# Kernel tuning notes

Measured on AMD Instinct MI355X. Metric: run time of the kernel, lower is better.

The kernel has to match this reference:

```python
import jax, jax.numpy as jnp
import numpy as np

N = 100000       # nodes
E = 3200000      # edges
IN_DIM = 128
EDGE_DIM = 16
H = 64           # hidden_dim
L = 3            # num_layers
G = 256          # num graphs
BN_EPS = 1e-5


def setup_inputs() -> dict:
    key = jax.random.key(0)
    ks = jax.random.split(key, 16)
    x = jax.random.normal(ks[0], (N, IN_DIM), dtype=jnp.float32)
    edge_attr = jax.random.normal(ks[1], (E, EDGE_DIM), dtype=jnp.float32)
    edge_index = jax.random.randint(ks[2], (2, E), 0, N, dtype=jnp.int64)
    batch = jnp.sort(jax.random.randint(ks[3], (N,), 0, G, dtype=jnp.int64))
    s = 0.05
    np_w = jax.random.normal(ks[4], (IN_DIM, H), dtype=jnp.float32) * s
    np_b = jnp.zeros((H,), dtype=jnp.float32)
    ep_w = jax.random.normal(ks[5], (EDGE_DIM, H), dtype=jnp.float32) * s
    ep_b = jnp.zeros((H,), dtype=jnp.float32)
    mlp_w1 = jax.random.normal(ks[6], (L, H, H), dtype=jnp.float32) * s
    mlp_b1 = jnp.zeros((L, H), dtype=jnp.float32)
    mlp_w2 = jax.random.normal(ks[7], (L, H, H), dtype=jnp.float32) * s
    mlp_b2 = jnp.zeros((L, H), dtype=jnp.float32)
    bn_g = jnp.ones((L, H), dtype=jnp.float32)
    bn_b = jnp.zeros((L, H), dtype=jnp.float32)
    return {"x": x, "edge_attr": edge_attr, "edge_index": edge_index, "batch": batch,
            "np_w": np_w, "np_b": np_b, "ep_w": ep_w, "ep_b": ep_b,
            "mlp_w1": mlp_w1, "mlp_b1": mlp_b1, "mlp_w2": mlp_w2, "mlp_b2": mlp_b2,
            "bn_g": bn_g, "bn_b": bn_b}


def reference(x, edge_attr, edge_index, batch, np_w, np_b, ep_w, ep_b,
              mlp_w1, mlp_b1, mlp_w2, mlp_b2, bn_g, bn_b):
    h = x @ np_w + np_b                  # [N,H] node_proj
    e = edge_attr @ ep_w + ep_b          # [E,H] edge_proj
    src, dst = edge_index[0], edge_index[1]
    for l in range(L):
        # GINEConv (eps=0): MLP(x_i + sum_j ReLU(x_j + e_ij))
        msg = jax.nn.relu(h[src] + e)                          # [E,H] gather + edge add
        agg = jax.ops.segment_sum(msg, dst, num_segments=N)    # scatter-add
        z = h + agg
        z = jax.nn.relu(z @ mlp_w1[l] + mlp_b1[l]) @ mlp_w2[l] + mlp_b2[l]
        # BatchNorm1d over node dim (batch statistics, training-mode math)
        mu = jnp.mean(z, axis=0)
        var = jnp.mean((z - mu) ** 2, axis=0)
        z = (z - mu) * jax.lax.rsqrt(var + BN_EPS) * bn_g[l] + bn_b[l]
        h = jax.nn.relu(z)               # dropout omitted (deterministic reference)
    # global_mean_pool
    sums = jax.ops.segment_sum(h, batch, num_segments=G)
    cnts = jax.ops.segment_sum(jnp.ones((N,), dtype=h.dtype), batch, num_segments=G)
    graph_emb = sums / jnp.maximum(cnts, 1.0)[:, None]
    return h, graph_emb
```

## Files before the change

kernel.cpp:

```cpp
#include <hip/hip_runtime.h>
#include <hip/hip_bf16.h>

#define NN 100000
#define NE 3200000
#define IND 128
#define ED 16
#define HD 64
#define NL 3
#define NG 256
#define BN_EPS 1e-5f

#define NB 391
#define PBLK 512
#define PCHUNK 6250
#define MLP_BLOCKS 2048
#define APPLY_BLOCKS 2048

typedef unsigned int uint32;
typedef unsigned long long uint64;
typedef unsigned short ushort16;

__device__ __forceinline__ ushort16 f2b(float f) {
    uint32 u = __float_as_uint(f);
    u = (u + 0x7fffu + ((u >> 16) & 1u)) >> 16;
    return (ushort16)u;
}
__device__ __forceinline__ float b2f(ushort16 b) {
    return __uint_as_float(((uint32)b) << 16);
}

__global__ __launch_bounds__(256) void k_node_proj(
    const float* __restrict__ x, const float* __restrict__ w,
    const float* __restrict__ b, ushort16* __restrict__ sb)
{
    __shared__ float xs[4][IND];
    const int wave = threadIdx.x >> 6, lane = threadIdx.x & 63;
    const int node = blockIdx.x * 4 + wave;
    const float2 v = *(const float2*)(x + (size_t)node * IND + lane * 2);
    ((float2*)xs[wave])[lane] = v;
    float acc = b[lane];
#pragma unroll
    for (int k = 0; k < IND; ++k)
        acc = fmaf(xs[wave][k], w[k * HD + lane], acc);
    sb[node * HD + lane] = f2b(acc);
}

__global__ __launch_bounds__(256) void k_p1(const int* __restrict__ ei,
                                            int* __restrict__ bh)
{
    __shared__ int hist[NB];
    const int t = threadIdx.x, blk = blockIdx.x;
    for (int i = t; i < NB; i += 256) hist[i] = 0;
    __syncthreads();
    const int base = blk * PCHUNK;
    for (int i = t; i < PCHUNK; i += 256)
        atomicAdd(&hist[ei[NE + base + i] >> 8], 1);
    __syncthreads();
    for (int i = t; i < NB; i += 256) bh[blk * NB + i] = hist[i];
}

__global__ __launch_bounds__(512) void k_p2(int* __restrict__ bh,
                                            int* __restrict__ bstart,
                                            int* __restrict__ rowptr)
{
    __shared__ int tot[NB];
    __shared__ int bsl[NB + 1];
    const int t = threadIdx.x;
    if (t < NB) {
        int s = 0;
        for (int blk = 0; blk < PBLK; ++blk) {
            const int idx = blk * NB + t;
            const int v = bh[idx];
            bh[idx] = s;
            s += v;
        }
        tot[t] = s;
    }
    __syncthreads();
    if (t == 0) {
        int run = 0;
        for (int b = 0; b < NB; ++b) { bsl[b] = run; run += tot[b]; }
        bsl[NB] = run;
    }
    __syncthreads();
    if (t < NB) {
        const int base = bsl[t];
        for (int blk = 0; blk < PBLK; ++blk) bh[blk * NB + t] += base;
        bstart[t] = base;
    }
    if (t == 0) { bstart[NB] = NE; rowptr[NN] = NE; }
}

__global__ __launch_bounds__(256) void k_p3(const int* __restrict__ ei,
                                            const int* __restrict__ bh,
                                            uint64* __restrict__ tmp)
{
    __shared__ int cursor[NB];
    const int t = threadIdx.x, blk = blockIdx.x;
    for (int i = t; i < NB; i += 256) cursor[i] = bh[blk * NB + i];
    __syncthreads();
    const int base = blk * PCHUNK;
    for (int i = t; i < PCHUNK; i += 256) {
        const int e = base + i;
        const int d = ei[NE + e];
        const int s = ei[e];
        const int pos = atomicAdd(&cursor[d >> 8], 1);
        tmp[pos] = (uint64)(uint32)d | ((uint64)(uint32)s << 17)
                 | ((uint64)(uint32)e << 34);
    }
}

__global__ __launch_bounds__(256) void k_p4(const uint64* __restrict__ tmp,
                                            const int* __restrict__ bstart,
                                            int2* __restrict__ perm_se,
                                            int* __restrict__ rowptr)
{
    __shared__ int cnt[256], csave[256], cnt2[256];
    const int t = threadIdx.x, b = blockIdx.x;
    const int lo = bstart[b], hi = bstart[b + 1];
    cnt[t] = 0; cnt2[t] = 0;
    __syncthreads();
    for (int e = lo + t; e < hi; e += 256)
        atomicAdd(&cnt[(int)(tmp[e] & 0x1FFFF) & 255], 1);
    __syncthreads();
    csave[t] = cnt[t];
    __syncthreads();
    for (int off = 1; off < 256; off <<= 1) {
        const int v = (t >= off) ? cnt[t - off] : 0;
        __syncthreads();
        cnt[t] += v;
        __syncthreads();
    }
    const int excl = cnt[t] - csave[t];
    const int node = (b << 8) + t;
    if (node < NN) rowptr[node] = lo + excl;
    __syncthreads();
    csave[t] = excl;
    __syncthreads();
    for (int e = lo + t; e < hi; e += 256) {
        const uint64 u = tmp[e];
        const int loc = (int)(u & 0x1FFFF) & 255;
        const int r = atomicAdd(&cnt2[loc], 1);
        const int pos = lo + csave[loc] + r;
        perm_se[pos] = make_int2((int)((u >> 17) & 0x1FFFF), (int)(u >> 34));
    }
}

__global__ __launch_bounds__(256) void k_permute(
    const float* __restrict__ ea, const int2* __restrict__ perm_se,
    ushort16* __restrict__ ea_perm)
{
    const int pos = blockIdx.x * 256 + threadIdx.x;
    const int p = pos >> 2, q = pos & 3;
    const int eid = perm_se[p].y;
    const float4 v = ((const float4*)(ea + (size_t)eid * ED))[q];
    ushort4 o;
    o.x = f2b(v.x); o.y = f2b(v.y); o.z = f2b(v.z); o.w = f2b(v.w);
    ((ushort4*)ea_perm)[pos] = o;
}

template <bool XFORM>
__global__ __launch_bounds__(256) void k_gather(
    const ushort16* __restrict__ eab, const int2* __restrict__ perm_se,
    const int* __restrict__ rowptr,
    const float* __restrict__ epw, const float* __restrict__ epb,
    const ushort16* __restrict__ sb, const float* __restrict__ bnp,
    float* __restrict__ z)
{
    const int lane = threadIdx.x & 63;
    float wr[ED];
#pragma unroll
    for (int k = 0; k < ED; ++k) wr[k] = epw[k * HD + lane];
    const float bc = epb[lane];
    const float tsc = XFORM ? bnp[lane] : 1.f;
    const float tsh = XFORM ? bnp[64 + lane] : 0.f;

    const int node = __builtin_amdgcn_readfirstlane((blockIdx.x << 2) + (threadIdx.x >> 6));
    const int rs = rowptr[node];
    const int re = rowptr[node + 1];

    float acc = 0.f;
    int j = rs;
    for (; j + 8 <= re; j += 8) {
        int s[8];
#pragma unroll
        for (int m = 0; m < 8; ++m) s[m] = perm_se[j + m].x;
        float hv[8];
#pragma unroll
        for (int m = 0; m < 8; ++m) {
            float v = b2f(sb[(size_t)s[m] * HD + lane]);
            if (XFORM) v = fmaxf(fmaf(v, tsc, tsh), 0.f);
            hv[m] = v;
        }
#pragma unroll
        for (int m = 0; m < 8; ++m) {
            const uint32* r = (const uint32*)(eab + (size_t)(j + m) * ED);
            float e = bc;
#pragma unroll
            for (int k2 = 0; k2 < ED / 2; ++k2) {
                const uint32 u = r[k2];
                e = fmaf(__uint_as_float(u << 16), wr[2 * k2], e);
                e = fmaf(__uint_as_float(u & 0xffff0000u), wr[2 * k2 + 1], e);
            }
            acc += fmaxf(hv[m] + e, 0.f);
        }
    }
    for (; j < re; ++j) {
        float v = b2f(sb[(size_t)perm_se[j].x * HD + lane]);
        if (XFORM) v = fmaxf(fmaf(v, tsc, tsh), 0.f);
        const uint32* r = (const uint32*)(eab + (size_t)j * ED);
        float e = bc;
#pragma unroll
        for (int k2 = 0; k2 < ED / 2; ++k2) {
            const uint32 u = r[k2];
            e = fmaf(__uint_as_float(u << 16), wr[2 * k2], e);
            e = fmaf(__uint_as_float(u & 0xffff0000u), wr[2 * k2 + 1], e);
        }
        acc += fmaxf(v + e, 0.f);
    }
    float u0 = b2f(sb[(size_t)node * HD + lane]);
    if (XFORM) u0 = fmaxf(fmaf(u0, tsc, tsh), 0.f);
    z[node * HD + lane] = acc + u0;
}

template <bool STORE_BF16>
__global__ __launch_bounds__(256) void k_mlp(
    float* __restrict__ z,
    const float* __restrict__ w1, const float* __restrict__ b1,
    const float* __restrict__ w2, const float* __restrict__ b2,
    ushort16* __restrict__ sb, float* __restrict__ part)
{
    __shared__ float z0s[4][HD];
    __shared__ float t1s[4][HD];
    __shared__ float red[4][2][HD];
    const int wave = threadIdx.x >> 6, lane = threadIdx.x & 63;
    const float vb1 = b1[lane], vb2 = b2[lane];
    float s1 = 0.f, s2 = 0.f;
    for (int node = blockIdx.x * 4 + wave; node < NN; node += MLP_BLOCKS * 4) {
        const int idx = node * HD + lane;
        z0s[wave][lane] = z[idx];
        float a = vb1;
#pragma unroll
        for (int k = 0; k < HD; ++k)
            a = fmaf(z0s[wave][k], w1[k * HD + lane], a);
        a = fmaxf(a, 0.f);
        t1s[wave][lane] = a;
        float o = vb2;
#pragma unroll
        for (int k = 0; k < HD; ++k)
            o = fmaf(t1s[wave][k], w2[k * HD + lane], o);
        if (STORE_BF16) sb[idx] = f2b(o);
        else            z[idx] = o;
        s1 += o;
        s2 += o * o;
    }
    red[wave][0][lane] = s1;
    red[wave][1][lane] = s2;
    __syncthreads();
    if (wave == 0) {
        float a = red[0][0][lane] + red[1][0][lane] + red[2][0][lane] + red[3][0][lane];
        float c = red[0][1][lane] + red[1][1][lane] + red[2][1][lane] + red[3][1][lane];
        part[blockIdx.x * 128 + lane] = a;
        part[blockIdx.x * 128 + 64 + lane] = c;
    }
}

__global__ __launch_bounds__(1024) void k_bn_final(
    const float* __restrict__ part,
    const float* __restrict__ g, const float* __restrict__ b,
    float* __restrict__ bnp)
{
    __shared__ float red[16][2][HD];
    const int c = threadIdx.x & 63;
    const int s = threadIdx.x >> 6;
    float s1 = 0.f, s2 = 0.f;
    for (int i = s; i < MLP_BLOCKS; i += 16) {
        s1 += part[i * 128 + c];
        s2 += part[i * 128 + 64 + c];
    }
    red[s][0][c] = s1;
    red[s][1][c] = s2;
    __syncthreads();
    if (s == 0) {
        float a = 0.f, q = 0.f;
#pragma unroll
        for (int i = 0; i < 16; ++i) { a += red[i][0][c]; q += red[i][1][c]; }
        const float mu  = a / (float)NN;
        const float var = q / (float)NN - mu * mu;
        const float rstd = rsqrtf(var + BN_EPS);
        const float sc = rstd * g[c];
        bnp[c] = sc;
        bnp[64 + c] = b[c] - mu * sc;
    }
}

__global__ __launch_bounds__(256) void k_bn_apply(
    const float* __restrict__ t2, const float* __restrict__ bnp,
    float* __restrict__ h)
{
    const int lane = threadIdx.x & 63;
    const float sc = bnp[lane];
    const float sh = bnp[64 + lane];
    int i = blockIdx.x * 256 + threadIdx.x;
    const int stride = APPLY_BLOCKS * 256;
    for (; i < NN * HD; i += stride)
        h[i] = fmaxf(t2[i] * sc + sh, 0.f);
}

__global__ __launch_bounds__(256) void k_pool(
    const float* __restrict__ h, const int* __restrict__ batch,
    float* __restrict__ emb)
{
    __shared__ float red[4][HD];
    const int g = blockIdx.x;
    const int lane = threadIdx.x & 63;
    const int wave = threadIdx.x >> 6;
    int lo = 0, hi = NN;
    while (lo < hi) { int m = (lo + hi) >> 1; if (batch[m] < g) lo = m + 1; else hi = m; }
    const int start = lo;
    hi = NN;
    while (lo < hi) { int m = (lo + hi) >> 1; if (batch[m] <= g) lo = m + 1; else hi = m; }
    const int end = lo;
    float acc = 0.f;
    for (int n = start + wave; n < end; n += 4) acc += h[(size_t)n * HD + lane];
    red[wave][lane] = acc;
    __syncthreads();
    if (wave == 0) {
        float a = red[0][lane] + red[1][lane] + red[2][lane] + red[3][lane];
        emb[g * HD + lane] = a / fmaxf((float)(end - start), 1.f);
    }
}

extern "C" void kernel_launch(void* const* d_in, const int* in_sizes, int n_in,
                              void* d_out, int out_size, void* d_ws, size_t ws_size,
                              hipStream_t stream)
{
    const float* x     = (const float*)d_in[0];
    const float* ea    = (const float*)d_in[1];
    const int*   ei    = (const int*)d_in[2];
    const int*   batch = (const int*)d_in[3];
    const float* np_w  = (const float*)d_in[4];
    const float* np_b  = (const float*)d_in[5];
    const float* ep_w  = (const float*)d_in[6];
    const float* ep_b  = (const float*)d_in[7];
    const float* w1    = (const float*)d_in[8];
    const float* b1    = (const float*)d_in[9];
    const float* w2    = (const float*)d_in[10];
    const float* b2    = (const float*)d_in[11];
    const float* bng   = (const float*)d_in[12];
    const float* bnb   = (const float*)d_in[13];

    float* h   = (float*)d_out;
    float* emb = h + (size_t)NN * HD;

    char* ws = (char*)d_ws;
    float*     agg     = (float*)    (ws);
    uint64*    tmp     = (uint64*)   (ws);
    float*     part    = (float*)    (ws + 25600000);
    float*     bnp     = (float*)    (ws + 26648576);
    int*       bh      = (int*)      (ws + 26650112);
    int*       bstart  = (int*)      (ws + 27450880);
    int*       rowptr  = (int*)      (ws + 27452448);
    ushort16*  sb      = (ushort16*) (ws + 27852464);
    int2*      perm_se = (int2*)     (ws + 40652464);
    ushort16*  ea_perm = (ushort16*) (ws + 66252464);

    k_node_proj<<<NN / 4, 256, 0, stream>>>(x, np_w, np_b, sb);

    k_p1<<<PBLK, 256, 0, stream>>>(ei, bh);
    k_p2<<<1, 512, 0, stream>>>(bh, bstart, rowptr);
    k_p3<<<PBLK, 256, 0, stream>>>(ei, bh, tmp);
    k_p4<<<NB, 256, 0, stream>>>(tmp, bstart, perm_se, rowptr);
    k_permute<<<NE * 4 / 256, 256, 0, stream>>>(ea, perm_se, ea_perm);

    for (int l = 0; l < NL; ++l) {
        if (l == 0)
            k_gather<false><<<NN / 4, 256, 0, stream>>>(
                ea_perm, perm_se, rowptr, ep_w, ep_b, sb, bnp, agg);
        else
            k_gather<true><<<NN / 4, 256, 0, stream>>>(
                ea_perm, perm_se, rowptr, ep_w, ep_b, sb, bnp + (l - 1) * 128, agg);
        if (l < NL - 1)
            k_mlp<true><<<MLP_BLOCKS, 256, 0, stream>>>(
                agg, w1 + l * HD * HD, b1 + l * HD, w2 + l * HD * HD, b2 + l * HD,
                sb, part);
        else
            k_mlp<false><<<MLP_BLOCKS, 256, 0, stream>>>(
                agg, w1 + l * HD * HD, b1 + l * HD, w2 + l * HD * HD, b2 + l * HD,
                sb, part);
        k_bn_final<<<1, 1024, 0, stream>>>(part, bng + l * HD, bnb + l * HD, bnp + l * 128);
    }

    k_bn_apply<<<APPLY_BLOCKS, 256, 0, stream>>>(agg, bnp + 2 * 128, h);
    k_pool<<<NG, 256, 0, stream>>>(h, batch, emb);
}
```

Before: 1.254 ms.

## Compute per-edge projection with bf16 MFMA and split perm into SoA arrays

The gather kernel now computes the 16-to-64 edge projection for 16 edges at a time with an MFMA 16x16x32 bf16 instruction, zero-padding K from 16 to 32, and stages the results through per-wave LDS so each lane reads its column. This replaces the per-lane scalar FMA loop of 16 multiply-adds per edge per lane. Separately, the interleaved (src,eid) int2 permutation is split into two int arrays, so gather reads only source indices and permute reads only edge ids. The change adds LDS traffic and clamped padded loads for partial tiles, and rounds the edge weights to bf16.

```diff
diff --git a/kernel.cpp b/kernel.cpp
--- a/kernel.cpp
+++ b/kernel.cpp
@@ -19,6 +19,8 @@
 typedef unsigned int uint32;
 typedef unsigned long long uint64;
 typedef unsigned short ushort16;
+typedef __attribute__((ext_vector_type(8))) short bf16x8;
+typedef __attribute__((ext_vector_type(4))) float f32x4;
 
 __device__ __forceinline__ ushort16 f2b(float f) {
     uint32 u = __float_as_uint(f);
@@ -112,7 +114,8 @@
 
 __global__ __launch_bounds__(256) void k_p4(const uint64* __restrict__ tmp,
                                             const int* __restrict__ bstart,
-                                            int2* __restrict__ perm_se,
+                                            int* __restrict__ perm_src,
+                                            int* __restrict__ perm_eid,
                                             int* __restrict__ rowptr)
 {
     __shared__ int cnt[256], csave[256], cnt2[256];
@@ -142,17 +145,18 @@
         const int loc = (int)(u & 0x1FFFF) & 255;
         const int r = atomicAdd(&cnt2[loc], 1);
         const int pos = lo + csave[loc] + r;
-        perm_se[pos] = make_int2((int)((u >> 17) & 0x1FFFF), (int)(u >> 34));
+        perm_src[pos] = (int)((u >> 17) & 0x1FFFF);
+        perm_eid[pos] = (int)(u >> 34);
     }
 }
 
 __global__ __launch_bounds__(256) void k_permute(
-    const float* __restrict__ ea, const int2* __restrict__ perm_se,
+    const float* __restrict__ ea, const int* __restrict__ perm_eid,
     ushort16* __restrict__ ea_perm)
 {
     const int pos = blockIdx.x * 256 + threadIdx.x;
     const int p = pos >> 2, q = pos & 3;
-    const int eid = perm_se[p].y;
+    const int eid = perm_eid[p];
     const float4 v = ((const float4*)(ea + (size_t)eid * ED))[q];
     ushort4 o;
     o.x = f2b(v.x); o.y = f2b(v.y); o.z = f2b(v.z); o.w = f2b(v.w);
@@ -161,62 +165,79 @@
 
 template <bool XFORM>
 __global__ __launch_bounds__(256) void k_gather(
-    const ushort16* __restrict__ eab, const int2* __restrict__ perm_se,
+    const ushort16* __restrict__ eab, const int* __restrict__ perm_src,
     const int* __restrict__ rowptr,
     const float* __restrict__ epw, const float* __restrict__ epb,
     const ushort16* __restrict__ sb, const float* __restrict__ bnp,
     float* __restrict__ z)
 {
+    __shared__ float pe[4][64 * 17];
     const int lane = threadIdx.x & 63;
-    float wr[ED];
-#pragma unroll
-    for (int k = 0; k < ED; ++k) wr[k] = epw[k * HD + lane];
+    const int wave = threadIdx.x >> 6;
+    const int l15 = lane & 15, lg = lane >> 4;
+
+    bf16x8 bfrag[4];
+#pragma unroll
+    for (int c = 0; c < 4; ++c) {
+#pragma unroll
+        for (int i = 0; i < 8; ++i) {
+            const int k = lg * 8 + i;
+            bfrag[c][i] = (k < ED) ? (short)f2b(epw[k * HD + c * 16 + l15])
+                                   : (short)0;
+        }
+    }
     const float bc = epb[lane];
     const float tsc = XFORM ? bnp[lane] : 1.f;
     const float tsh = XFORM ? bnp[64 + lane] : 0.f;
-
-    const int node = __builtin_amdgcn_readfirstlane((blockIdx.x << 2) + (threadIdx.x >> 6));
+    float* mype = pe[wave];
+
+    const int node = __builtin_amdgcn_readfirstlane((blockIdx.x << 2) + wave);
     const int rs = rowptr[node];
     const int re = rowptr[node + 1];
 
     float acc = 0.f;
-    int j = rs;
-    for (; j + 8 <= re; j += 8) {
-        int s[8];
-#pragma unroll
-        for (int m = 0; m < 8; ++m) s[m] = perm_se[j + m].x;
-        float hv[8];
-#pragma unroll
-        for (int m = 0; m < 8; ++m) {
-            float v = b2f(sb[(size_t)s[m] * HD + lane]);
-            if (XFORM) v = fmaxf(fmaf(v, tsc, tsh), 0.f);
-            hv[m] = v;
+    for (int j = rs; j < re; j += 16) {
+        bf16x8 a = {};
+        if (lg < 2) {
+            int row = j + l15;
+            if (row > NE - 1) row = NE - 1;
+            a = *(const bf16x8*)((const short*)eab + (size_t)row * ED + lg * 8);
         }
-#pragma unroll
-        for (int m = 0; m < 8; ++m) {
-            const uint32* r = (const uint32*)(eab + (size_t)(j + m) * ED);
-            float e = bc;
-#pragma unroll
-            for (int k2 = 0; k2 < ED / 2; ++k2) {
-                const uint32 u = r[k2];
-                e = fmaf(__uint_as_float(u << 16), wr[2 * k2], e);
-                e = fmaf(__uint_as_float(u & 0xffff0000u), wr[2 * k2 + 1], e);
+        const f32x4 zero = {0.f, 0.f, 0.f, 0.f};
+#pragma unroll
+        for (int c = 0; c < 4; ++c) {
+            const f32x4 d = __builtin_amdgcn_mfma_f32_16x16x32_bf16(
+                a, bfrag[c], zero, 0, 0, 0);
+            const int base = (c * 16 + l15) * 17 + lg * 4;
+#pragma unroll
+            for (int v = 0; v < 4; ++v) mype[base + v] = d[v];
+        }
+#pragma unroll
+        for (int half = 0; half < 2; ++half) {
+            const int jb = j + half * 8;
+            int s[8];
+#pragma unroll
+            for (int m = 0; m < 8; ++m) {
+                int idx = jb + m;
+                if (idx > NE - 1) idx = NE - 1;
+                s[m] = perm_src[idx];
             }
-            acc += fmaxf(hv[m] + e, 0.f);
+            float hv[8];
+#pragma unroll
+            for (int m = 0; m < 8; ++m) {
+                float v = b2f(sb[(size_t)s[m] * HD + lane]);
+                if (XFORM) v = fmaxf(fmaf(v, tsc, tsh), 0.f);
+                hv[m] = v;
+            }
+            const int lim = re - jb;
+#pragma unroll
+            for (int m = 0; m < 8; ++m) {
+                if (m < lim) {
+                    const float e = mype[lane * 17 + half * 8 + m] + bc;
+                    acc += fmaxf(hv[m] + e, 0.f);
+                }
+            }
         }
-    }
-    for (; j < re; ++j) {
-        float v = b2f(sb[(size_t)perm_se[j].x * HD + lane]);
-        if (XFORM) v = fmaxf(fmaf(v, tsc, tsh), 0.f);
-        const uint32* r = (const uint32*)(eab + (size_t)j * ED);
-        float e = bc;
-#pragma unroll
-        for (int k2 = 0; k2 < ED / 2; ++k2) {
-            const uint32 u = r[k2];
-            e = fmaf(__uint_as_float(u << 16), wr[2 * k2], e);
-            e = fmaf(__uint_as_float(u & 0xffff0000u), wr[2 * k2 + 1], e);
-        }
-        acc += fmaxf(v + e, 0.f);
     }
     float u0 = b2f(sb[(size_t)node * HD + lane]);
     if (XFORM) u0 = fmaxf(fmaf(u0, tsc, tsh), 0.f);
@@ -354,32 +375,33 @@
     float* emb = h + (size_t)NN * HD;
 
     char* ws = (char*)d_ws;
-    float*     agg     = (float*)    (ws);
-    uint64*    tmp     = (uint64*)   (ws);
-    float*     part    = (float*)    (ws + 25600000);
-    float*     bnp     = (float*)    (ws + 26648576);
-    int*       bh      = (int*)      (ws + 26650112);
-    int*       bstart  = (int*)      (ws + 27450880);
-    int*       rowptr  = (int*)      (ws + 27452448);
-    ushort16*  sb      = (ushort16*) (ws + 27852464);
-    int2*      perm_se = (int2*)     (ws + 40652464);
-    ushort16*  ea_perm = (ushort16*) (ws + 66252464);
+    float*     agg      = (float*)    (ws);
+    uint64*    tmp      = (uint64*)   (ws);
+    float*     part     = (float*)    (ws + 25600000);
+    float*     bnp      = (float*)    (ws + 26648576);
+    int*       bh       = (int*)      (ws + 26650112);
+    int*       bstart   = (int*)      (ws + 27450880);
+    int*       rowptr   = (int*)      (ws + 27452448);
+    ushort16*  sb       = (ushort16*) (ws + 27852464);
+    int*       perm_src = (int*)      (ws + 40652464);
+    int*       perm_eid = (int*)      (ws + 53452464);
+    ushort16*  ea_perm  = (ushort16*) (ws + 66252464);
 
     k_node_proj<<<NN / 4, 256, 0, stream>>>(x, np_w, np_b, sb);
 
     k_p1<<<PBLK, 256, 0, stream>>>(ei, bh);
     k_p2<<<1, 512, 0, stream>>>(bh, bstart, rowptr);
     k_p3<<<PBLK, 256, 0, stream>>>(ei, bh, tmp);
-    k_p4<<<NB, 256, 0, stream>>>(tmp, bstart, perm_se, rowptr);
-    k_permute<<<NE * 4 / 256, 256, 0, stream>>>(ea, perm_se, ea_perm);
+    k_p4<<<NB, 256, 0, stream>>>(tmp, bstart, perm_src, perm_eid, rowptr);
+    k_permute<<<NE * 4 / 256, 256, 0, stream>>>(ea, perm_eid, ea_perm);
 
     for (int l = 0; l < NL; ++l) {
         if (l == 0)
             k_gather<false><<<NN / 4, 256, 0, stream>>>(
-                ea_perm, perm_se, rowptr, ep_w, ep_b, sb, bnp, agg);
+                ea_perm, perm_src, rowptr, ep_w, ep_b, sb, bnp, agg);
         else
             k_gather<true><<<NN / 4, 256, 0, stream>>>(
-                ea_perm, perm_se, rowptr, ep_w, ep_b, sb, bnp + (l - 1) * 128, agg);
+                ea_perm, perm_src, rowptr, ep_w, ep_b, sb, bnp + (l - 1) * 128, agg);
         if (l < NL - 1)
             k_mlp<true><<<MLP_BLOCKS, 256, 0, stream>>>(
                 agg, w1 + l * HD * HD, b1 + l * HD, w2 + l * HD * HD, b2 + l * HD,
```

Result: slower. 1.301 ms (+3.7%).
